# Kernel tuning notes

Hardware: AMD Instinct MI355X
Metric: run time of the kernel (lower is better)

Reference implementation:

```python
import jax, jax.numpy as jnp
import numpy as np

B, S, A, M, H, OUT = 256, 256, 256, 256, 8, 256
KD = A // H   # key_dim per head = 32
VD = M // H   # value_dim per head = 32


def setup_inputs() -> dict:
    key = jax.random.key(0)
    ks = jax.random.split(key, 11)
    return {
        "q_data": jax.random.normal(ks[0], (B, S, A), dtype=jnp.float32),
        "m_data": jax.random.normal(ks[1], (B, S, M), dtype=jnp.float32),
        "bias": jax.random.normal(ks[2], (B, 1, 1, S), dtype=jnp.float32),
        "nonbatched_bias": jax.random.normal(ks[3], (H, S, S), dtype=jnp.float32),
        "query_w": jax.random.normal(ks[4], (A, H, KD), dtype=jnp.float32) * 0.05,
        "key_w": jax.random.normal(ks[5], (M, H, KD), dtype=jnp.float32) * 0.05,
        "value_w": jax.random.normal(ks[6], (M, H, VD), dtype=jnp.float32) * 0.05,
        "gating_w": jax.random.normal(ks[7], (A, H, VD), dtype=jnp.float32) * 0.05,
        "gating_b": jax.random.normal(ks[8], (H, VD), dtype=jnp.float32) * 0.05,
        "output_w": jax.random.normal(ks[9], (H, VD, OUT), dtype=jnp.float32) * 0.05,
        "output_b": jax.random.normal(ks[10], (OUT,), dtype=jnp.float32) * 0.05,
    }


def reference(q_data, m_data, bias, nonbatched_bias,
              query_w, key_w, value_w, gating_w, gating_b, output_w, output_b):
    key_dim = query_w.shape[-1]
    # projections
    q = jnp.einsum('bqa,ahc->bqhc', q_data, query_w) * key_dim ** (-0.5)
    k = jnp.einsum('bka,ahc->bkhc', m_data, key_w)
    v = jnp.einsum('bka,ahc->bkhc', m_data, value_w)
    # logits [b,h,q,k] with batched + shared bias
    logits = jnp.einsum('bqhc,bkhc->bhqk', q, k) + bias + nonbatched_bias[None]
    weights = jax.nn.softmax(logits, axis=-1)
    weighted_avg = jnp.einsum('bhqk,bkhc->bqhc', weights, v)
    # sigmoid gating
    gate_values = jax.nn.sigmoid(jnp.einsum('bqc,chv->bqhv', q_data, gating_w) + gating_b)
    weighted_avg = weighted_avg * gate_values
    # output projection
    output = jnp.einsum('bqhc,hco->bqo', weighted_avg, output_w) + output_b
    return output
```

## Files before the change

kernel.cpp:

```cpp
#include <hip/hip_runtime.h>

typedef unsigned short u16;
typedef __attribute__((ext_vector_type(8))) short short8;
typedef __attribute__((ext_vector_type(4))) float f32x4;
typedef __attribute__((ext_vector_type(4))) unsigned int u32x4;
typedef __attribute__((ext_vector_type(4))) unsigned short u16x4;

#define LOG2E 1.4426950408889634f

__device__ __forceinline__ float bf2f(u16 u) {
    union { float f; unsigned int i; } c; c.i = ((unsigned int)u) << 16; return c.f;
}
__device__ __forceinline__ u16 f2bf(float f) {
    unsigned int x = __float_as_uint(f);
    x += 0x7fff + ((x >> 16) & 1);
    return (u16)(x >> 16);
}

union Cvt32 { u32x4 v[4]; u16 u[32]; };

__device__ __forceinline__ void ld32f_bf(const float* __restrict__ p, Cvt32& t) {
#pragma unroll
    for (int j = 0; j < 32; j += 4) {
        f32x4 x = *(const f32x4*)(p + j);
        t.u[j]     = f2bf(x[0]);
        t.u[j + 1] = f2bf(x[1]);
        t.u[j + 2] = f2bf(x[2]);
        t.u[j + 3] = f2bf(x[3]);
    }
}


__global__ __launch_bounds__(256) void prep_a(
    const float* __restrict__ nb,
    const float* __restrict__ qw, const float* __restrict__ kw,
    const float* __restrict__ vw, const float* __restrict__ gw,
    const float* __restrict__ ow,
    u16* __restrict__ wt, u16* __restrict__ WoT, u16* __restrict__ nbT)
{
    __shared__ float tile[64][65];
    int blk = blockIdx.x, tid = threadIdx.x;
    if (blk < 1024) {
        int e = blk * 256 + tid;
        int n = e & 255, k = (e >> 8) & 255, g = e >> 16;
        const float* W = g == 0 ? kw : g == 1 ? vw : g == 2 ? qw : gw;
        wt[(((g << 8) | n) << 8) | k] = f2bf(W[k * 256 + n]);
    } else if (blk < 1280) {
        int e = (blk - 1024) * 256 + tid;
        int o = e & 255, hc = e >> 8;
        WoT[o * 256 + hc] = f2bf(ow[hc * 256 + o]);
    } else {
        int idx = blk - 1280;
        int q0 = (idx & 3) * 64, k0 = ((idx >> 2) & 3) * 64, h = idx >> 4;
        int rr = tid >> 4;
        int cc = (tid & 15) << 2;
        const float* src = nb + ((size_t)(h * 256 + q0)) * 256 + k0;
#pragma unroll
        for (int p = 0; p < 4; p++) {
            int q = rr + p * 16;
            f32x4 x = *(const f32x4*)(src + (size_t)q * 256 + cc);
            tile[q][cc] = x[0]; tile[q][cc + 1] = x[1];
            tile[q][cc + 2] = x[2]; tile[q][cc + 3] = x[3];
        }
        __syncthreads();
        u16* dst = nbT + ((size_t)(h * 256 + k0)) * 256 + q0;
#pragma unroll
        for (int p = 0; p < 4; p++) {
            int k = rr + p * 16;
            u16x4 o;
#pragma unroll
            for (int u = 0; u < 4; u++) o[u] = f2bf(tile[cc + u][k] * LOG2E);
            *(u16x4*)(dst + (size_t)k * 256 + cc) = o;
        }
    }
}

__global__ __launch_bounds__(256) void proj_a(
    const float* __restrict__ m_data, const float* __restrict__ q_data,
    const u16* __restrict__ wt,
    u16* __restrict__ Kh, u16* __restrict__ Vh, u16* __restrict__ Qh,
    u16* __restrict__ GW, const float* __restrict__ gb)
{
    __shared__ u16 As[128 * 40];
    __shared__ u16 Bs[128 * 40];
    int bid = blockIdx.x;
    int xcd = bid & 7;
    int slot = bid >> 3;
    int y = slot & 7;
    int x = ((slot >> 3) << 3) | xcd;
    int row0 = x * 128;
    int n0 = y * 128;
    int g = y >> 1;
    const float* X = (g < 2) ? m_data : q_data;

    int tid = threadIdx.x;
    int lane = tid & 63, w = tid >> 6;
    int wm = w >> 1, wn = w & 1;
    int lr = tid >> 1;
    int lc = (tid & 1) << 4;

    const f32x4 fz = {0.f, 0.f, 0.f, 0.f};
    f32x4 acc[4][4];
#pragma unroll
    for (int i = 0; i < 4; i++)
#pragma unroll
        for (int j = 0; j < 4; j++) acc[i][j] = fz;

    int kl = (lane >> 4) << 3;
    int l15 = lane & 15;
    int rm = wm * 64 + l15;
    int rn = wn * 64 + l15;

    for (int kb = 0; kb < 8; ++kb) {
        int k0 = kb << 5;
        const float* pa = X + (size_t)(row0 + lr) * 256 + k0 + lc;
        f32x4 x0 = *(const f32x4*)pa;
        f32x4 x1 = *(const f32x4*)(pa + 4);
        f32x4 x2 = *(const f32x4*)(pa + 8);
        f32x4 x3 = *(const f32x4*)(pa + 12);
        union { u32x4 v[2]; u16 u[16]; } am;
        am.u[0] = f2bf(x0[0]); am.u[1] = f2bf(x0[1]); am.u[2] = f2bf(x0[2]); am.u[3] = f2bf(x0[3]);
        am.u[4] = f2bf(x1[0]); am.u[5] = f2bf(x1[1]); am.u[6] = f2bf(x1[2]); am.u[7] = f2bf(x1[3]);
        am.u[8] = f2bf(x2[0]); am.u[9] = f2bf(x2[1]); am.u[10] = f2bf(x2[2]); am.u[11] = f2bf(x2[3]);
        am.u[12] = f2bf(x3[0]); am.u[13] = f2bf(x3[1]); am.u[14] = f2bf(x3[2]); am.u[15] = f2bf(x3[3]);
        const u16* pb = wt + ((size_t)(n0 + lr) << 8) + k0 + lc;
        u32x4 b0 = *(const u32x4*)pb;
        u32x4 b1 = *(const u32x4*)(pb + 8);
        if (kb) __syncthreads();
        *(u32x4*)&As[lr * 40 + lc] = am.v[0];
        *(u32x4*)&As[lr * 40 + lc + 8] = am.v[1];
        *(u32x4*)&Bs[lr * 40 + lc] = b0;
        *(u32x4*)&Bs[lr * 40 + lc + 8] = b1;
        __syncthreads();
        short8 af[4], bf[4];
#pragma unroll
        for (int i = 0; i < 4; i++) af[i] = *(const short8*)&As[(rm + i * 16) * 40 + kl];
#pragma unroll
        for (int i = 0; i < 4; i++) bf[i] = *(const short8*)&Bs[(rn + i * 16) * 40 + kl];
#pragma unroll
        for (int mi = 0; mi < 4; mi++)
#pragma unroll
            for (int ni = 0; ni < 4; ni++)
                acc[mi][ni] = __builtin_amdgcn_mfma_f32_16x16x32_bf16(af[mi], bf[ni], acc[mi][ni], 0, 0, 0);
    }

    u16* dst = (g == 0) ? Kh : (g == 1) ? Vh : (g == 2) ? Qh : GW;
    float scale = (g == 2) ? 0.17677669529663687f * LOG2E : 1.f;
#pragma unroll
    for (int mi = 0; mi < 4; mi++)
#pragma unroll
        for (int ni = 0; ni < 4; ni++)
#pragma unroll
            for (int r = 0; r < 4; r++) {
                int row = row0 + wm * 64 + mi * 16 + ((lane >> 4) << 2) + r;
                int col = n0 + wn * 64 + ni * 16 + l15;
                float v = acc[mi][ni][r] * scale;
                int hc = col & 255;
                if (g == 3) v = (v + gb[hc]) * LOG2E;
                int b = row >> 8, s = row & 255, h = hc >> 5, c = col & 31;
                dst[((((size_t)b * 8 + h) << 8) + s) * 32 + c] = f2bf(v);
            }
}

__global__ __launch_bounds__(256, 3) void attn_a(
    const u16* __restrict__ Qh, const u16* __restrict__ Kh,
    const u16* __restrict__ Vh, u16* GW,
    const float* __restrict__ bias2, const u16* __restrict__ nbT)
{
    __shared__ u16 smem[23296];
    u16* Ksh = smem;
    u16* Vt  = smem + 10240;
    int bid = blockIdx.x;
    int b = bid >> 3, h = bid & 7;
    int tid = threadIdx.x, lane = tid & 63, w = tid >> 6;
    int l15 = lane & 15;
    int kl = (lane >> 4) << 3;
    int rq = (lane >> 4) << 2;
    size_t hoff = ((size_t)(b * 8 + h)) << 13;
    const f32x4 fz = {0.f, 0.f, 0.f, 0.f};
    u16* myP = smem + 18688 + w * 1152;

    {
        const u16* p = Kh + hoff + (tid << 5);
        u32x4 v0 = *(const u32x4*)p,        v1 = *(const u32x4*)(p + 8);
        u32x4 v2 = *(const u32x4*)(p + 16), v3 = *(const u32x4*)(p + 24);
        *(u32x4*)&Ksh[tid * 40] = v0;      *(u32x4*)&Ksh[tid * 40 + 8] = v1;
        *(u32x4*)&Ksh[tid * 40 + 16] = v2; *(u32x4*)&Ksh[tid * 40 + 24] = v3;
    }
    {
        const u16* p = Vh + hoff + (tid << 5);
        Cvt32 tm;
        tm.v[0] = *(const u32x4*)p;        tm.v[1] = *(const u32x4*)(p + 8);
        tm.v[2] = *(const u32x4*)(p + 16); tm.v[3] = *(const u32x4*)(p + 24);
#pragma unroll
        for (int c = 0; c < 32; c++) Vt[c * 264 + tid] = tm.u[c];
    }
    float bload[16];
#pragma unroll
    for (int t = 0; t < 16; t++)
        bload[t] = bias2[(b << 8) + t * 16 + l15] * LOG2E;
    __syncthreads();

    short8 kf[16];
#pragma unroll
    for (int t = 0; t < 16; t++) kf[t] = *(const short8*)&Ksh[(t * 16 + l15) * 40 + kl];

    const u16* nbh = nbT + ((size_t)h << 16);
    int orow = lane >> 2, ocol = (lane & 3) << 3;

#pragma unroll 1
    for (int mt = 0; mt < 4; ++mt) {
        int q0 = 64 * w + mt * 16 + rq;
        short8 qf = *(const short8*)(Qh + hoff + (size_t)(64 * w + mt * 16 + l15) * 32 + kl);

        size_t gaddr = hoff + (size_t)(64 * w + mt * 16 + orow) * 32 + ocol;
        u32x4 gl = *(const u32x4*)(GW + gaddr);

        const u16* nbp = nbh + q0;
        float srow[4] = {0.f, 0.f, 0.f, 0.f};
        f32x4 oacc[2] = {fz, fz};
#pragma unroll
        for (int qt = 0; qt < 4; ++qt) {
            f32x4 sc[4];
#pragma unroll
            for (int t = 0; t < 4; t++) {
                int tt = qt * 4 + t;
                f32x4 cb = {bload[tt], bload[tt], bload[tt], bload[tt]};
                sc[t] = __builtin_amdgcn_mfma_f32_16x16x32_bf16(qf, kf[tt], cb, 0, 0, 0);
            }
#pragma unroll
            for (int t = 0; t < 4; t++) {
                int tt = qt * 4 + t;
                u16x4 nbv = *(const u16x4*)(nbp + ((tt * 16 + l15) << 8));
#pragma unroll
                for (int r = 0; r < 4; r++) {
                    float p = __builtin_amdgcn_exp2f(sc[t][r] + bf2f(nbv[r]));
                    srow[r] += p;
                    myP[(rq + r) * 72 + t * 16 + l15] = f2bf(p);
                }
            }
#pragma unroll
            for (int ks = 0; ks < 2; ++ks) {
                short8 pf = *(const short8*)&myP[l15 * 72 + ks * 32 + kl];
#pragma unroll
                for (int ni = 0; ni < 2; ++ni) {
                    short8 vf = *(const short8*)&Vt[(ni * 16 + l15) * 264 + qt * 64 + ks * 32 + kl];
                    oacc[ni] = __builtin_amdgcn_mfma_f32_16x16x32_bf16(pf, vf, oacc[ni], 0, 0, 0);
                }
            }
        }
#pragma unroll
        for (int r = 0; r < 4; r++) {
            float s = srow[r];
            s += __shfl_xor(s, 1);
            s += __shfl_xor(s, 2);
            s += __shfl_xor(s, 4);
            s += __shfl_xor(s, 8);
            srow[r] = __builtin_amdgcn_rcpf(s);
        }

#pragma unroll
        for (int ni = 0; ni < 2; ++ni)
#pragma unroll
            for (int r = 0; r < 4; r++)
                myP[(rq + r) * 40 + ni * 16 + l15] = f2bf(oacc[ni][r] * srow[r]);
        u32x4 ov = *(const u32x4*)&myP[orow * 40 + ocol];
        union { u32x4 v; u16 u[8]; } oi, gi, oo;
        oi.v = ov; gi.v = gl;
#pragma unroll
        for (int j = 0; j < 8; j++) {
            float gate = __builtin_amdgcn_rcpf(1.f + __builtin_amdgcn_exp2f(-bf2f(gi.u[j])));
            oo.u[j] = f2bf(bf2f(oi.u[j]) * gate);
        }
        *(u32x4*)(GW + gaddr) = oo.v;
    }
}

__global__ __launch_bounds__(256) void gemmout_a(
    const u16* __restrict__ WA, const u16* __restrict__ WoT,
    float* __restrict__ dst, const float* __restrict__ ob)
{
    __shared__ u16 As[128 * 40];
    __shared__ u16 Bs[128 * 40];
    int tid = threadIdx.x;
    int lane = tid & 63, w = tid >> 6;
    int wm = w >> 1, wn = w & 1;
    int row0 = blockIdx.x * 128;
    int n0 = blockIdx.y * 128;
    int bq = row0 >> 8, s0 = row0 & 255;
    int lr = tid >> 1;
    int lc = (tid & 1) << 4;

    const f32x4 fz = {0.f, 0.f, 0.f, 0.f};
    f32x4 acc[4][4];
#pragma unroll
    for (int i = 0; i < 4; i++)
#pragma unroll
        for (int j = 0; j < 4; j++) acc[i][j] = fz;

    int kl = (lane >> 4) << 3;
    int l15 = lane & 15;
    int rm = wm * 64 + l15;
    int rn = wn * 64 + l15;

    for (int kb = 0; kb < 8; ++kb) {
        int k0 = kb << 5;
        const u16* pa = WA + ((((size_t)bq * 8 + kb) << 8) + s0 + lr) * 32 + lc;
        u32x4 a0 = *(const u32x4*)pa;
        u32x4 a1 = *(const u32x4*)(pa + 8);
        const u16* pb = WoT + ((size_t)(n0 + lr) << 8) + k0 + lc;
        u32x4 b0 = *(const u32x4*)pb;
        u32x4 b1 = *(const u32x4*)(pb + 8);
        if (kb) __syncthreads();
        *(u32x4*)&As[lr * 40 + lc] = a0;
        *(u32x4*)&As[lr * 40 + lc + 8] = a1;
        *(u32x4*)&Bs[lr * 40 + lc] = b0;
        *(u32x4*)&Bs[lr * 40 + lc + 8] = b1;
        __syncthreads();
        short8 af[4], bf[4];
#pragma unroll
        for (int i = 0; i < 4; i++) af[i] = *(const short8*)&As[(rm + i * 16) * 40 + kl];
#pragma unroll
        for (int i = 0; i < 4; i++) bf[i] = *(const short8*)&Bs[(rn + i * 16) * 40 + kl];
#pragma unroll
        for (int mi = 0; mi < 4; mi++)
#pragma unroll
            for (int ni = 0; ni < 4; ni++)
                acc[mi][ni] = __builtin_amdgcn_mfma_f32_16x16x32_bf16(af[mi], bf[ni], acc[mi][ni], 0, 0, 0);
    }

#pragma unroll
    for (int mi = 0; mi < 4; mi++)
#pragma unroll
        for (int ni = 0; ni < 4; ni++)
#pragma unroll
            for (int r = 0; r < 4; r++) {
                int row = row0 + wm * 64 + mi * 16 + ((lane >> 4) << 2) + r;
                int col = n0 + wn * 64 + ni * 16 + l15;
                dst[((size_t)row << 8) + col] = acc[mi][ni][r] + ob[col];
            }
}


__global__ __launch_bounds__(256) void transpose_k(
    const float* __restrict__ query_w, const float* __restrict__ key_w,
    const float* __restrict__ value_w, const float* __restrict__ gating_w,
    u16* __restrict__ wt)
{
    int i = blockIdx.x * 256 + threadIdx.x;
    int half = i >> 17;
    int rem = i & 131071;
    int h = rem >> 14, e = rem & 16383;
    int n = e >> 8, k = e & 255;
    int src_idx = k * 256 + h * 32 + (n & 31);
    float v;
    if (half == 0) v = (n < 32) ? key_w[src_idx]   : value_w[src_idx];
    else           v = (n < 32) ? query_w[src_idx] : gating_w[src_idx];
    wt[i] = f2bf(v);
}

__global__ __launch_bounds__(256) void fused_attn_k(
    const float* __restrict__ q_data, const float* __restrict__ m_data,
    const float* __restrict__ bias2, const float* __restrict__ nb,
    const u16* __restrict__ wt, const float* __restrict__ gb,
    u16* __restrict__ WAo)
{
    __shared__ u16 smem[31488];
    u16* Ksh = smem;
    u16* Vt  = smem + 10240;
    u16* Xs  = smem + 18688;
    u16* Wsh = smem + 28928;

    int bid = blockIdx.x;
    int b = bid >> 3, h = bid & 7;
    int tid = threadIdx.x, lane = tid & 63, w = tid >> 6;
    int l15 = lane & 15;
    int kl = (lane >> 4) << 3;
    int rq = (lane >> 4) << 2;
    const f32x4 fz = {0.f, 0.f, 0.f, 0.f};

    float bload[16];
#pragma unroll
    for (int t = 0; t < 16; t++) bload[t] = bias2[(b << 8) + t * 16 + l15];
    float gbc0 = gb[h * 32 + l15];
    float gbc1 = gb[h * 32 + 16 + l15];

    const float* Xg = m_data + ((size_t)b << 16);
    const u16* Wg = wt + (h << 14);
    f32x4 acc[4][4];
#pragma unroll
    for (int i = 0; i < 4; i++)
#pragma unroll
        for (int j = 0; j < 4; j++) acc[i][j] = fz;

    for (int kb = 0; kb < 8; ++kb) {
        Cvt32 am;
        ld32f_bf(Xg + (size_t)tid * 256 + kb * 32, am);
        u32x4 b0, b1;
        int nrow = tid >> 1, nc = (tid & 1) << 4;
        if (tid < 128) {
            const u16* q = Wg + nrow * 256 + kb * 32 + nc;
            b0 = *(const u32x4*)q; b1 = *(const u32x4*)(q + 8);
        }
        if (kb) __syncthreads();
        *(u32x4*)&Xs[tid * 40]      = am.v[0];
        *(u32x4*)&Xs[tid * 40 + 8]  = am.v[1];
        *(u32x4*)&Xs[tid * 40 + 16] = am.v[2];
        *(u32x4*)&Xs[tid * 40 + 24] = am.v[3];
        if (tid < 128) {
            *(u32x4*)&Wsh[nrow * 40 + nc] = b0;
            *(u32x4*)&Wsh[nrow * 40 + nc + 8] = b1;
        }
        __syncthreads();
        short8 af[4], bf[4];
#pragma unroll
        for (int i = 0; i < 4; i++) af[i] = *(const short8*)&Xs[(64 * w + i * 16 + l15) * 40 + kl];
#pragma unroll
        for (int i = 0; i < 4; i++) bf[i] = *(const short8*)&Wsh[(i * 16 + l15) * 40 + kl];
#pragma unroll
        for (int mi = 0; mi < 4; mi++)
#pragma unroll
            for (int ni = 0; ni < 4; ni++)
                acc[mi][ni] = __builtin_amdgcn_mfma_f32_16x16x32_bf16(af[mi], bf[ni], acc[mi][ni], 0, 0, 0);
    }
#pragma unroll
    for (int mi = 0; mi < 4; mi++)
#pragma unroll
        for (int ni = 0; ni < 4; ni++)
#pragma unroll
            for (int r = 0; r < 4; r++) {
                int s = 64 * w + mi * 16 + rq + r;
                int col = ni * 16 + l15;
                u16 v = f2bf(acc[mi][ni][r]);
                if (ni < 2) Ksh[s * 40 + col] = v;
                else        Vt[(col - 32) * 264 + s] = v;
            }
    __syncthreads();

    const float* Xg2 = q_data + ((size_t)b << 16);
    const u16* Wg2 = wt + 131072 + (h << 14);
    f32x4 acc2[4][4];
#pragma unroll
    for (int i = 0; i < 4; i++)
#pragma unroll
        for (int j = 0; j < 4; j++) acc2[i][j] = fz;

    for (int kb = 0; kb < 8; ++kb) {
        Cvt32 am;
        ld32f_bf(Xg2 + (size_t)tid * 256 + kb * 32, am);
        u32x4 b0, b1;
        int nrow = tid >> 1, nc = (tid & 1) << 4;
        if (tid < 128) {
            const u16* q = Wg2 + nrow * 256 + kb * 32 + nc;
            b0 = *(const u32x4*)q; b1 = *(const u32x4*)(q + 8);
        }
        __syncthreads();
        *(u32x4*)&Xs[tid * 40]      = am.v[0];
        *(u32x4*)&Xs[tid * 40 + 8]  = am.v[1];
        *(u32x4*)&Xs[tid * 40 + 16] = am.v[2];
        *(u32x4*)&Xs[tid * 40 + 24] = am.v[3];
        if (tid < 128) {
            *(u32x4*)&Wsh[nrow * 40 + nc] = b0;
            *(u32x4*)&Wsh[nrow * 40 + nc + 8] = b1;
        }
        __syncthreads();
        short8 af[4], bf[4];
#pragma unroll
        for (int i = 0; i < 4; i++) af[i] = *(const short8*)&Xs[(64 * w + i * 16 + l15) * 40 + kl];
#pragma unroll
        for (int i = 0; i < 4; i++) bf[i] = *(const short8*)&Wsh[(i * 16 + l15) * 40 + kl];
#pragma unroll
        for (int mi = 0; mi < 4; mi++)
#pragma unroll
            for (int ni = 0; ni < 4; ni++)
                acc2[mi][ni] = __builtin_amdgcn_mfma_f32_16x16x32_bf16(af[mi], bf[ni], acc2[mi][ni], 0, 0, 0);
    }
    __syncthreads();

    u16* myQ = smem + 18688 + w * 2816;
    u16* myP = myQ + 640;
    const float* nbp = nb + ((size_t)h << 16);
    const float qscale = 0.17677669529663687f;

#pragma unroll 1
    for (int mt = 0; mt < 4; ++mt) {
#pragma unroll
        for (int ni = 0; ni < 2; ++ni)
#pragma unroll
            for (int r = 0; r < 4; r++)
                myQ[(rq + r) * 40 + ni * 16 + l15] = f2bf(acc2[mt][ni][r] * qscale);

        short8 qf = *(const short8*)&myQ[l15 * 40 + kl];
        f32x4 sc[16];
#pragma unroll
        for (int t = 0; t < 16; t++) {
            short8 kfr = *(const short8*)&Ksh[(t * 16 + l15) * 40 + kl];
            sc[t] = __builtin_amdgcn_mfma_f32_16x16x32_bf16(qf, kfr, fz, 0, 0, 0);
        }

        int q0 = 64 * w + mt * 16 + rq;
        float mrow[4] = {-3e30f, -3e30f, -3e30f, -3e30f};
#pragma unroll
        for (int t = 0; t < 16; t++) {
            int kidx = t * 16 + l15;
#pragma unroll
            for (int r = 0; r < 4; r++) {
                float v = sc[t][r] + bload[t] + nbp[(size_t)(q0 + r) * 256 + kidx];
                sc[t][r] = v;
                mrow[r] = fmaxf(mrow[r], v);
            }
        }
#pragma unroll
        for (int r = 0; r < 4; r++) {
            float m = mrow[r];
            m = fmaxf(m, __shfl_xor(m, 1));
            m = fmaxf(m, __shfl_xor(m, 2));
            m = fmaxf(m, __shfl_xor(m, 4));
            m = fmaxf(m, __shfl_xor(m, 8));
            mrow[r] = m;
        }
        float srow[4] = {0.f, 0.f, 0.f, 0.f};
#pragma unroll
        for (int t = 0; t < 16; t++)
#pragma unroll
            for (int r = 0; r < 4; r++) {
                float p = __expf(sc[t][r] - mrow[r]);
                sc[t][r] = p;
                srow[r] += p;
            }
#pragma unroll
        for (int r = 0; r < 4; r++) {
            float s = srow[r];
            s += __shfl_xor(s, 1);
            s += __shfl_xor(s, 2);
            s += __shfl_xor(s, 4);
            s += __shfl_xor(s, 8);
            srow[r] = 1.f / s;
        }

        f32x4 oacc[2] = {fz, fz};
#pragma unroll
        for (int half = 0; half < 2; ++half) {
#pragma unroll
            for (int t = 0; t < 8; t++)
#pragma unroll
                for (int r = 0; r < 4; r++)
                    myP[(rq + r) * 136 + t * 16 + l15] =
                        f2bf(sc[half * 8 + t][r] * srow[r]);
#pragma unroll
            for (int ks = 0; ks < 4; ++ks) {
                short8 pf = *(const short8*)&myP[l15 * 136 + ks * 32 + kl];
#pragma unroll
                for (int ni = 0; ni < 2; ++ni) {
                    short8 vf = *(const short8*)&Vt[(ni * 16 + l15) * 264 + half * 128 + ks * 32 + kl];
                    oacc[ni] = __builtin_amdgcn_mfma_f32_16x16x32_bf16(pf, vf, oacc[ni], 0, 0, 0);
                }
            }
        }

#pragma unroll
        for (int ni = 0; ni < 2; ++ni) {
            float gbv = ni ? gbc1 : gbc0;
#pragma unroll
            for (int r = 0; r < 4; r++) {
                float gate = 1.f / (1.f + __expf(-(acc2[mt][ni + 2][r] + gbv)));
                size_t idx = (((size_t)b << 8) + q0 + r) * 256 + h * 32 + ni * 16 + l15;
                WAo[idx] = f2bf(oacc[ni][r] * gate);
            }
        }
    }
}

__global__ __launch_bounds__(256) void gemm_out_k(
    const u16* __restrict__ X, const float* __restrict__ Wo,
    float* __restrict__ dst, const float* __restrict__ cbias)
{
    __shared__ u16 As[128 * 40];
    __shared__ u16 Bs[128 * 40];
    int tid = threadIdx.x;
    int lane = tid & 63, w = tid >> 6;
    int wm = w >> 1, wn = w & 1;
    int row0 = blockIdx.x * 128;
    int n0 = blockIdx.y * 128;
    int lr = tid >> 1;
    int lc = (tid & 1) << 4;

    const f32x4 fz = {0.f, 0.f, 0.f, 0.f};
    f32x4 acc[4][4];
#pragma unroll
    for (int i = 0; i < 4; i++)
#pragma unroll
        for (int j = 0; j < 4; j++) acc[i][j] = fz;

    int kl = (lane >> 4) << 3;
    int l15 = lane & 15;
    int rm = wm * 64 + l15;
    int rn = wn * 64 + l15;

    for (int kb = 0; kb < 8; ++kb) {
        int k0 = kb << 5;
        const u16* pa = X + ((size_t)(row0 + lr) << 8) + k0 + lc;
        u32x4 a0 = *(const u32x4*)pa;
        u32x4 a1 = *(const u32x4*)(pa + 8);
        int bk = tid >> 3, bn = (tid & 7) << 4;
        const float* pb = Wo + (size_t)(k0 + bk) * 256 + n0 + bn;
        u16 bu[16];
#pragma unroll
        for (int j = 0; j < 16; j += 4) {
            f32x4 x = *(const f32x4*)(pb + j);
            bu[j] = f2bf(x[0]); bu[j + 1] = f2bf(x[1]);
            bu[j + 2] = f2bf(x[2]); bu[j + 3] = f2bf(x[3]);
        }
        if (kb) __syncthreads();
        *(u32x4*)&As[lr * 40 + lc] = a0;
        *(u32x4*)&As[lr * 40 + lc + 8] = a1;
#pragma unroll
        for (int j = 0; j < 16; j++) Bs[(bn + j) * 40 + bk] = bu[j];
        __syncthreads();
        short8 af[4], bf[4];
#pragma unroll
        for (int i = 0; i < 4; i++) af[i] = *(const short8*)&As[(rm + i * 16) * 40 + kl];
#pragma unroll
        for (int i = 0; i < 4; i++) bf[i] = *(const short8*)&Bs[(rn + i * 16) * 40 + kl];
#pragma unroll
        for (int mi = 0; mi < 4; mi++)
#pragma unroll
            for (int ni = 0; ni < 4; ni++)
                acc[mi][ni] = __builtin_amdgcn_mfma_f32_16x16x32_bf16(af[mi], bf[ni], acc[mi][ni], 0, 0, 0);
    }

#pragma unroll
    for (int mi = 0; mi < 4; mi++)
#pragma unroll
        for (int ni = 0; ni < 4; ni++)
#pragma unroll
            for (int r = 0; r < 4; r++) {
                int row = row0 + wm * 64 + mi * 16 + ((lane >> 4) << 2) + r;
                int col = n0 + wn * 64 + ni * 16 + l15;
                dst[((size_t)row << 8) + col] = acc[mi][ni][r] + cbias[col];
            }
}

extern "C" void kernel_launch(void* const* d_in, const int* in_sizes, int n_in,
                              void* d_out, int out_size, void* d_ws, size_t ws_size,
                              hipStream_t stream)
{
    const float* q_data   = (const float*)d_in[0];
    const float* m_data   = (const float*)d_in[1];
    const float* bias     = (const float*)d_in[2];
    const float* nb       = (const float*)d_in[3];
    const float* query_w  = (const float*)d_in[4];
    const float* key_w    = (const float*)d_in[5];
    const float* value_w  = (const float*)d_in[6];
    const float* gating_w = (const float*)d_in[7];
    const float* gating_b = (const float*)d_in[8];
    const float* output_w = (const float*)d_in[9];
    const float* output_b = (const float*)d_in[10];

    const size_t NEED_A = 4ull * 33554432 + 524288 + 131072 + 1048576;

    if (ws_size >= NEED_A) {
        u16* ws   = (u16*)d_ws;
        u16* Kh   = ws;
        u16* Vh   = Kh + 16777216;
        u16* Qh   = Vh + 16777216;
        u16* GW   = Qh + 16777216;
        u16* wt   = GW + 16777216;
        u16* WoT  = wt + 262144;
        u16* nbT  = WoT + 65536;

        prep_a<<<1408, 256, 0, stream>>>(nb, query_w, key_w, value_w, gating_w,
                                         output_w, wt, WoT, nbT);
        proj_a<<<4096, 256, 0, stream>>>(m_data, q_data, wt, Kh, Vh, Qh, GW, gating_b);
        attn_a<<<2048, 256, 0, stream>>>(Qh, Kh, Vh, GW, bias, nbT);
        gemmout_a<<<dim3(512, 2), 256, 0, stream>>>(GW, WoT, (float*)d_out, output_b);
    } else {
        u16* WAb = (u16*)d_ws;
        u16* wt  = (u16*)d_out;
        transpose_k<<<1024, 256, 0, stream>>>(query_w, key_w, value_w, gating_w, wt);
        fused_attn_k<<<2048, 256, 0, stream>>>(q_data, m_data, bias, nb, wt, gating_b, WAb);
        gemm_out_k<<<dim3(512, 2), 256, 0, stream>>>(WAb, output_w, (float*)d_out, output_b);
    }
}
```

Baseline: 441.9 us.

## Widen proj GEMM K-step, use packed bf16 convert, stage epilogue via LDS

The projection GEMM kernel now loads 64-wide K slices per iteration (4 iterations instead of 8), halving the barriers. The fp32-to-bf16 conversion of activations uses the packed v_cvt_pk_bf16_f32 instruction instead of manual rounding. The output epilogue writes results into shared memory first, then emits coalesced 16-byte stores per head row instead of scattered 2-byte stores. This cuts global store transactions and ALU work, at the cost of more LDS usage (36KB), which may lower occupancy.

```diff
diff --git a/kernel.cpp b/kernel.cpp
--- a/kernel.cpp
+++ b/kernel.cpp
@@ -15,6 +15,11 @@
     unsigned int x = __float_as_uint(f);
     x += 0x7fff + ((x >> 16) & 1);
     return (u16)(x >> 16);
+}
+__device__ __forceinline__ unsigned int cvtpk(float lo, float hi) {
+    unsigned int d;
+    asm("v_cvt_pk_bf16_f32 %0, %1, %2" : "=v"(d) : "v"(lo), "v"(hi));
+    return d;
 }
 
 union Cvt32 { u32x4 v[4]; u16 u[32]; };
@@ -81,8 +86,9 @@
     u16* __restrict__ Kh, u16* __restrict__ Vh, u16* __restrict__ Qh,
     u16* __restrict__ GW, const float* __restrict__ gb)
 {
-    __shared__ u16 As[128 * 40];
-    __shared__ u16 Bs[128 * 40];
+    __shared__ u16 smem[18432];
+    u16* As = smem;
+    u16* Bs = smem + 9216;
     int bid = blockIdx.x;
     int xcd = bid & 7;
     int slot = bid >> 3;
@@ -97,7 +103,7 @@
     int lane = tid & 63, w = tid >> 6;
     int wm = w >> 1, wn = w & 1;
     int lr = tid >> 1;
-    int lc = (tid & 1) << 4;
+    int lc2 = (tid & 1) << 5;
 
     const f32x4 fz = {0.f, 0.f, 0.f, 0.f};
     f32x4 acc[4][4];
@@ -108,58 +114,87 @@
 
     int kl = (lane >> 4) << 3;
     int l15 = lane & 15;
+    int rq = (lane >> 4) << 2;
     int rm = wm * 64 + l15;
     int rn = wn * 64 + l15;
 
-    for (int kb = 0; kb < 8; ++kb) {
-        int k0 = kb << 5;
-        const float* pa = X + (size_t)(row0 + lr) * 256 + k0 + lc;
-        f32x4 x0 = *(const f32x4*)pa;
-        f32x4 x1 = *(const f32x4*)(pa + 4);
-        f32x4 x2 = *(const f32x4*)(pa + 8);
-        f32x4 x3 = *(const f32x4*)(pa + 12);
-        union { u32x4 v[2]; u16 u[16]; } am;
-        am.u[0] = f2bf(x0[0]); am.u[1] = f2bf(x0[1]); am.u[2] = f2bf(x0[2]); am.u[3] = f2bf(x0[3]);
-        am.u[4] = f2bf(x1[0]); am.u[5] = f2bf(x1[1]); am.u[6] = f2bf(x1[2]); am.u[7] = f2bf(x1[3]);
-        am.u[8] = f2bf(x2[0]); am.u[9] = f2bf(x2[1]); am.u[10] = f2bf(x2[2]); am.u[11] = f2bf(x2[3]);
-        am.u[12] = f2bf(x3[0]); am.u[13] = f2bf(x3[1]); am.u[14] = f2bf(x3[2]); am.u[15] = f2bf(x3[3]);
-        const u16* pb = wt + ((size_t)(n0 + lr) << 8) + k0 + lc;
+    for (int kb = 0; kb < 4; ++kb) {
+        int k0 = kb << 6;
+        const float* pa = X + (size_t)(row0 + lr) * 256 + k0 + lc2;
+        union { u32x4 v[2]; unsigned int i[8]; } a0, a1;
+#pragma unroll
+        for (int j = 0; j < 4; j++) {
+            f32x4 xx = *(const f32x4*)(pa + j * 4);
+            a0.i[j * 2]     = cvtpk(xx[0], xx[1]);
+            a0.i[j * 2 + 1] = cvtpk(xx[2], xx[3]);
+        }
+#pragma unroll
+        for (int j = 0; j < 4; j++) {
+            f32x4 xx = *(const f32x4*)(pa + 16 + j * 4);
+            a1.i[j * 2]     = cvtpk(xx[0], xx[1]);
+            a1.i[j * 2 + 1] = cvtpk(xx[2], xx[3]);
+        }
+        const u16* pb = wt + ((size_t)(n0 + lr) << 8) + k0 + lc2;
         u32x4 b0 = *(const u32x4*)pb;
         u32x4 b1 = *(const u32x4*)(pb + 8);
+        u32x4 b2 = *(const u32x4*)(pb + 16);
+        u32x4 b3 = *(const u32x4*)(pb + 24);
         if (kb) __syncthreads();
-        *(u32x4*)&As[lr * 40 + lc] = am.v[0];
-        *(u32x4*)&As[lr * 40 + lc + 8] = am.v[1];
-        *(u32x4*)&Bs[lr * 40 + lc] = b0;
-        *(u32x4*)&Bs[lr * 40 + lc + 8] = b1;
+        *(u32x4*)&As[lr * 72 + lc2]      = a0.v[0];
+        *(u32x4*)&As[lr * 72 + lc2 + 8]  = a0.v[1];
+        *(u32x4*)&As[lr * 72 + lc2 + 16] = a1.v[0];
+        *(u32x4*)&As[lr * 72 + lc2 + 24] = a1.v[1];
+        *(u32x4*)&Bs[lr * 72 + lc2]      = b0;
+        *(u32x4*)&Bs[lr * 72 + lc2 + 8]  = b1;
+        *(u32x4*)&Bs[lr * 72 + lc2 + 16] = b2;
+        *(u32x4*)&Bs[lr * 72 + lc2 + 24] = b3;
         __syncthreads();
-        short8 af[4], bf[4];
-#pragma unroll
-        for (int i = 0; i < 4; i++) af[i] = *(const short8*)&As[(rm + i * 16) * 40 + kl];
-#pragma unroll
-        for (int i = 0; i < 4; i++) bf[i] = *(const short8*)&Bs[(rn + i * 16) * 40 + kl];
-#pragma unroll
-        for (int mi = 0; mi < 4; mi++)
-#pragma unroll
-            for (int ni = 0; ni < 4; ni++)
-                acc[mi][ni] = __builtin_amdgcn_mfma_f32_16x16x32_bf16(af[mi], bf[ni], acc[mi][ni], 0, 0, 0);
+#pragma unroll
+        for (int ks = 0; ks < 2; ++ks) {
+            short8 af[4], bf[4];
+#pragma unroll
+            for (int i = 0; i < 4; i++) af[i] = *(const short8*)&As[(rm + i * 16) * 72 + ks * 32 + kl];
+#pragma unroll
+            for (int i = 0; i < 4; i++) bf[i] = *(const short8*)&Bs[(rn + i * 16) * 72 + ks * 32 + kl];
+#pragma unroll
+            for (int mi = 0; mi < 4; mi++)
+#pragma unroll
+                for (int ni = 0; ni < 4; ni++)
+                    acc[mi][ni] = __builtin_amdgcn_mfma_f32_16x16x32_bf16(af[mi], bf[ni], acc[mi][ni], 0, 0, 0);
+        }
     }
 
     u16* dst = (g == 0) ? Kh : (g == 1) ? Vh : (g == 2) ? Qh : GW;
     float scale = (g == 2) ? 0.17677669529663687f * LOG2E : 1.f;
+
+    __syncthreads();
+    u16* Cs = smem;
 #pragma unroll
     for (int mi = 0; mi < 4; mi++)
 #pragma unroll
         for (int ni = 0; ni < 4; ni++)
 #pragma unroll
             for (int r = 0; r < 4; r++) {
-                int row = row0 + wm * 64 + mi * 16 + ((lane >> 4) << 2) + r;
-                int col = n0 + wn * 64 + ni * 16 + l15;
+                int row = wm * 64 + mi * 16 + rq + r;
+                int col = wn * 64 + ni * 16 + l15;
                 float v = acc[mi][ni][r] * scale;
-                int hc = col & 255;
-                if (g == 3) v = (v + gb[hc]) * LOG2E;
-                int b = row >> 8, s = row & 255, h = hc >> 5, c = col & 31;
-                dst[((((size_t)b * 8 + h) << 8) + s) * 32 + c] = f2bf(v);
-            }
+                if (g == 3) v = (v + gb[((y & 1) << 7) + col]) * LOG2E;
+                Cs[row * 136 + col] = f2bf(v);
+            }
+    __syncthreads();
+    {
+        int b = row0 >> 8, s0 = row0 & 255;
+        int hh = ((y & 1) << 2) | w;
+        u16* dstp = dst + ((((size_t)b * 8 + hh) << 8) + s0) * 32;
+        int ls = lane >> 2;
+        int lcc = (lane & 3) << 3;
+#pragma unroll
+        for (int p = 0; p < 8; p++) {
+            int s = p * 16 + ls;
+            u32x4 vv = *(const u32x4*)&Cs[s * 136 + w * 32 + lcc];
+            *(u32x4*)(dstp + (size_t)s * 32 + lcc) = vv;
+        }
+    }
 }
 
 __global__ __launch_bounds__(256, 3) void attn_a(
```

Result: slower. 463.8 us (+5.0%).

## Load MFMA fragments directly from global memory in projection and output GEMMs

Applied to the files above, without the earlier changes.

The projection and output GEMM kernels no longer stage A/B tiles through shared memory with two barriers per k-step. Each wave now loads its MFMA operand fragments straight from global memory, relying on L1/L2 for the reuse between waves. The fp32-to-bf16 conversion uses the packed v_cvt_pk_bf16_f32 instruction instead of manual rounding. This removes the LDS traffic and synchronisation, but each element is fetched by more waves and the global access pattern is less coalesced.

```diff
diff --git a/kernel.cpp b/kernel.cpp
--- a/kernel.cpp
+++ b/kernel.cpp
@@ -15,6 +15,11 @@
     unsigned int x = __float_as_uint(f);
     x += 0x7fff + ((x >> 16) & 1);
     return (u16)(x >> 16);
+}
+__device__ __forceinline__ unsigned int cvtpk(float lo, float hi) {
+    unsigned int d;
+    asm("v_cvt_pk_bf16_f32 %0, %1, %2" : "=v"(d) : "v"(lo), "v"(hi));
+    return d;
 }
 
 union Cvt32 { u32x4 v[4]; u16 u[32]; };
@@ -81,8 +86,6 @@
     u16* __restrict__ Kh, u16* __restrict__ Vh, u16* __restrict__ Qh,
     u16* __restrict__ GW, const float* __restrict__ gb)
 {
-    __shared__ u16 As[128 * 40];
-    __shared__ u16 Bs[128 * 40];
     int bid = blockIdx.x;
     int xcd = bid & 7;
     int slot = bid >> 3;
@@ -96,8 +99,6 @@
     int tid = threadIdx.x;
     int lane = tid & 63, w = tid >> 6;
     int wm = w >> 1, wn = w & 1;
-    int lr = tid >> 1;
-    int lc = (tid & 1) << 4;
 
     const f32x4 fz = {0.f, 0.f, 0.f, 0.f};
     f32x4 acc[4][4];
@@ -108,35 +109,29 @@
 
     int kl = (lane >> 4) << 3;
     int l15 = lane & 15;
-    int rm = wm * 64 + l15;
-    int rn = wn * 64 + l15;
-
+    int rq = (lane >> 4) << 2;
+
+    const float* pa = X + (size_t)(row0 + wm * 64 + l15) * 256 + kl;
+    const u16*   pb = wt + (size_t)(n0 + wn * 64 + l15) * 256 + kl;
+
+#pragma unroll 1
     for (int kb = 0; kb < 8; ++kb) {
         int k0 = kb << 5;
-        const float* pa = X + (size_t)(row0 + lr) * 256 + k0 + lc;
-        f32x4 x0 = *(const f32x4*)pa;
-        f32x4 x1 = *(const f32x4*)(pa + 4);
-        f32x4 x2 = *(const f32x4*)(pa + 8);
-        f32x4 x3 = *(const f32x4*)(pa + 12);
-        union { u32x4 v[2]; u16 u[16]; } am;
-        am.u[0] = f2bf(x0[0]); am.u[1] = f2bf(x0[1]); am.u[2] = f2bf(x0[2]); am.u[3] = f2bf(x0[3]);
-        am.u[4] = f2bf(x1[0]); am.u[5] = f2bf(x1[1]); am.u[6] = f2bf(x1[2]); am.u[7] = f2bf(x1[3]);
-        am.u[8] = f2bf(x2[0]); am.u[9] = f2bf(x2[1]); am.u[10] = f2bf(x2[2]); am.u[11] = f2bf(x2[3]);
-        am.u[12] = f2bf(x3[0]); am.u[13] = f2bf(x3[1]); am.u[14] = f2bf(x3[2]); am.u[15] = f2bf(x3[3]);
-        const u16* pb = wt + ((size_t)(n0 + lr) << 8) + k0 + lc;
-        u32x4 b0 = *(const u32x4*)pb;
-        u32x4 b1 = *(const u32x4*)(pb + 8);
-        if (kb) __syncthreads();
-        *(u32x4*)&As[lr * 40 + lc] = am.v[0];
-        *(u32x4*)&As[lr * 40 + lc + 8] = am.v[1];
-        *(u32x4*)&Bs[lr * 40 + lc] = b0;
-        *(u32x4*)&Bs[lr * 40 + lc + 8] = b1;
-        __syncthreads();
         short8 af[4], bf[4];
 #pragma unroll
-        for (int i = 0; i < 4; i++) af[i] = *(const short8*)&As[(rm + i * 16) * 40 + kl];
-#pragma unroll
-        for (int i = 0; i < 4; i++) bf[i] = *(const short8*)&Bs[(rn + i * 16) * 40 + kl];
+        for (int i = 0; i < 4; i++) {
+            f32x4 x0 = *(const f32x4*)(pa + (size_t)i * 16 * 256 + k0);
+            f32x4 x1 = *(const f32x4*)(pa + (size_t)i * 16 * 256 + k0 + 4);
+            union { unsigned int i4[4]; short8 s; } c;
+            c.i4[0] = cvtpk(x0[0], x0[1]);
+            c.i4[1] = cvtpk(x0[2], x0[3]);
+            c.i4[2] = cvtpk(x1[0], x1[1]);
+            c.i4[3] = cvtpk(x1[2], x1[3]);
+            af[i] = c.s;
+        }
+#pragma unroll
+        for (int i = 0; i < 4; i++)
+            bf[i] = *(const short8*)(pb + (size_t)i * 16 * 256 + k0);
 #pragma unroll
         for (int mi = 0; mi < 4; mi++)
 #pragma unroll
@@ -152,7 +147,7 @@
         for (int ni = 0; ni < 4; ni++)
 #pragma unroll
             for (int r = 0; r < 4; r++) {
-                int row = row0 + wm * 64 + mi * 16 + ((lane >> 4) << 2) + r;
+                int row = row0 + wm * 64 + mi * 16 + rq + r;
                 int col = n0 + wn * 64 + ni * 16 + l15;
                 float v = acc[mi][ni][r] * scale;
                 int hc = col & 255;
@@ -280,16 +275,12 @@
     const u16* __restrict__ WA, const u16* __restrict__ WoT,
     float* __restrict__ dst, const float* __restrict__ ob)
 {
-    __shared__ u16 As[128 * 40];
-    __shared__ u16 Bs[128 * 40];
     int tid = threadIdx.x;
     int lane = tid & 63, w = tid >> 6;
     int wm = w >> 1, wn = w & 1;
     int row0 = blockIdx.x * 128;
     int n0 = blockIdx.y * 128;
     int bq = row0 >> 8, s0 = row0 & 255;
-    int lr = tid >> 1;
-    int lc = (tid & 1) << 4;
 
     const f32x4 fz = {0.f, 0.f, 0.f, 0.f};
     f32x4 acc[4][4];
@@ -300,28 +291,20 @@
 
     int kl = (lane >> 4) << 3;
     int l15 = lane & 15;
-    int rm = wm * 64 + l15;
-    int rn = wn * 64 + l15;
-
+    int rq = (lane >> 4) << 2;
+
+    const u16* pb = WoT + (size_t)(n0 + wn * 64 + l15) * 256 + kl;
+
+#pragma unroll 1
     for (int kb = 0; kb < 8; ++kb) {
-        int k0 = kb << 5;
-        const u16* pa = WA + ((((size_t)bq * 8 + kb) << 8) + s0 + lr) * 32 + lc;
-        u32x4 a0 = *(const u32x4*)pa;
-        u32x4 a1 = *(const u32x4*)(pa + 8);
-        const u16* pb = WoT + ((size_t)(n0 + lr) << 8) + k0 + lc;
-        u32x4 b0 = *(const u32x4*)pb;
-        u32x4 b1 = *(const u32x4*)(pb + 8);
-        if (kb) __syncthreads();
-        *(u32x4*)&As[lr * 40 + lc] = a0;
-        *(u32x4*)&As[lr * 40 + lc + 8] = a1;
-        *(u32x4*)&Bs[lr * 40 + lc] = b0;
-        *(u32x4*)&Bs[lr * 40 + lc + 8] = b1;
-        __syncthreads();
         short8 af[4], bf[4];
 #pragma unroll
-        for (int i = 0; i < 4; i++) af[i] = *(const short8*)&As[(rm + i * 16) * 40 + kl];
-#pragma unroll
-        for (int i = 0; i < 4; i++) bf[i] = *(const short8*)&Bs[(rn + i * 16) * 40 + kl];
+        for (int i = 0; i < 4; i++)
+            af[i] = *(const short8*)(WA +
+                (((size_t)bq * 8 + kb) * 256 + s0 + wm * 64 + i * 16 + l15) * 32 + kl);
+#pragma unroll
+        for (int i = 0; i < 4; i++)
+            bf[i] = *(const short8*)(pb + (size_t)i * 16 * 256 + kb * 32);
 #pragma unroll
         for (int mi = 0; mi < 4; mi++)
 #pragma unroll
@@ -335,7 +318,7 @@
         for (int ni = 0; ni < 4; ni++)
 #pragma unroll
             for (int r = 0; r < 4; r++) {
-                int row = row0 + wm * 64 + mi * 16 + ((lane >> 4) << 2) + r;
+                int row = row0 + wm * 64 + mi * 16 + rq + r;
                 int col = n0 + wn * 64 + ni * 16 + l15;
                 dst[((size_t)row << 8) + col] = acc[mi][ni][r] + ob[col];
             }
```

After: 556.0 us. 1.26x slower.

## Stage full activation row-block in LDS once and reuse across four output tiles

Applied to the files above, without the earlier changes.

The projection kernel now loads a 128x256 slab of m_data or q_data once, converts it to bf16 with the packed v_cvt_pk_bf16_f32 instruction, and keeps it in LDS. It then loops over four 128-column output tiles, reading weight fragments directly from global memory. Before, each of the 4096 blocks re-read and re-converted its activation slice, so every fp32 input row was fetched four times. The grid drops to 1024 blocks and LDS use grows to about 66 KB per block, which reduces occupancy, and the weight loads move from LDS staging to direct global reads with no double buffering.

```diff
diff --git a/kernel.cpp b/kernel.cpp
--- a/kernel.cpp
+++ b/kernel.cpp
@@ -15,6 +15,11 @@
     unsigned int x = __float_as_uint(f);
     x += 0x7fff + ((x >> 16) & 1);
     return (u16)(x >> 16);
+}
+__device__ __forceinline__ unsigned int cvtpk(float lo, float hi) {
+    unsigned int d;
+    asm("v_cvt_pk_bf16_f32 %0, %1, %2" : "=v"(d) : "v"(lo), "v"(hi));
+    return d;
 }
 
 union Cvt32 { u32x4 v[4]; u16 u[32]; };
@@ -81,85 +86,84 @@
     u16* __restrict__ Kh, u16* __restrict__ Vh, u16* __restrict__ Qh,
     u16* __restrict__ GW, const float* __restrict__ gb)
 {
-    __shared__ u16 As[128 * 40];
-    __shared__ u16 Bs[128 * 40];
+    __shared__ u16 As[128 * 264];
     int bid = blockIdx.x;
-    int xcd = bid & 7;
-    int slot = bid >> 3;
-    int y = slot & 7;
-    int x = ((slot >> 3) << 3) | xcd;
+    int x = bid >> 1;
+    int src = bid & 1;
     int row0 = x * 128;
-    int n0 = y * 128;
-    int g = y >> 1;
-    const float* X = (g < 2) ? m_data : q_data;
+    const float* X = src ? q_data : m_data;
 
     int tid = threadIdx.x;
     int lane = tid & 63, w = tid >> 6;
     int wm = w >> 1, wn = w & 1;
-    int lr = tid >> 1;
-    int lc = (tid & 1) << 4;
-
-    const f32x4 fz = {0.f, 0.f, 0.f, 0.f};
-    f32x4 acc[4][4];
-#pragma unroll
-    for (int i = 0; i < 4; i++)
-#pragma unroll
-        for (int j = 0; j < 4; j++) acc[i][j] = fz;
-
     int kl = (lane >> 4) << 3;
     int l15 = lane & 15;
+    int rq = (lane >> 4) << 2;
+
+    {
+        const float* base = X + (size_t)row0 * 256;
+#pragma unroll
+        for (int it = 0; it < 32; ++it) {
+            int fi = (it * 256 + tid) * 4;
+            int row = fi >> 8, col = fi & 255;
+            f32x4 xx = *(const f32x4*)(base + fi);
+            union { unsigned int i2[2]; u16x4 s; } c;
+            c.i2[0] = cvtpk(xx[0], xx[1]);
+            c.i2[1] = cvtpk(xx[2], xx[3]);
+            *(u16x4*)&As[row * 264 + col] = c.s;
+        }
+    }
+    __syncthreads();
+
+    const f32x4 fz = {0.f, 0.f, 0.f, 0.f};
     int rm = wm * 64 + l15;
-    int rn = wn * 64 + l15;
-
-    for (int kb = 0; kb < 8; ++kb) {
-        int k0 = kb << 5;
-        const float* pa = X + (size_t)(row0 + lr) * 256 + k0 + lc;
-        f32x4 x0 = *(const f32x4*)pa;
-        f32x4 x1 = *(const f32x4*)(pa + 4);
-        f32x4 x2 = *(const f32x4*)(pa + 8);
-        f32x4 x3 = *(const f32x4*)(pa + 12);
-        union { u32x4 v[2]; u16 u[16]; } am;
-        am.u[0] = f2bf(x0[0]); am.u[1] = f2bf(x0[1]); am.u[2] = f2bf(x0[2]); am.u[3] = f2bf(x0[3]);
-        am.u[4] = f2bf(x1[0]); am.u[5] = f2bf(x1[1]); am.u[6] = f2bf(x1[2]); am.u[7] = f2bf(x1[3]);
-        am.u[8] = f2bf(x2[0]); am.u[9] = f2bf(x2[1]); am.u[10] = f2bf(x2[2]); am.u[11] = f2bf(x2[3]);
-        am.u[12] = f2bf(x3[0]); am.u[13] = f2bf(x3[1]); am.u[14] = f2bf(x3[2]); am.u[15] = f2bf(x3[3]);
-        const u16* pb = wt + ((size_t)(n0 + lr) << 8) + k0 + lc;
-        u32x4 b0 = *(const u32x4*)pb;
-        u32x4 b1 = *(const u32x4*)(pb + 8);
-        if (kb) __syncthreads();
-        *(u32x4*)&As[lr * 40 + lc] = am.v[0];
-        *(u32x4*)&As[lr * 40 + lc + 8] = am.v[1];
-        *(u32x4*)&Bs[lr * 40 + lc] = b0;
-        *(u32x4*)&Bs[lr * 40 + lc + 8] = b1;
-        __syncthreads();
-        short8 af[4], bf[4];
-#pragma unroll
-        for (int i = 0; i < 4; i++) af[i] = *(const short8*)&As[(rm + i * 16) * 40 + kl];
-#pragma unroll
-        for (int i = 0; i < 4; i++) bf[i] = *(const short8*)&Bs[(rn + i * 16) * 40 + kl];
+
+#pragma unroll 1
+    for (int nt = 0; nt < 4; ++nt) {
+        int n0 = src * 512 + nt * 128;
+        int g  = n0 >> 8;
+        const u16* pb = wt + (size_t)(n0 + wn * 64 + l15) * 256 + kl;
+
+        f32x4 acc[4][4];
+#pragma unroll
+        for (int i = 0; i < 4; i++)
+#pragma unroll
+            for (int j = 0; j < 4; j++) acc[i][j] = fz;
+
+#pragma unroll
+        for (int kb = 0; kb < 8; ++kb) {
+            int k0 = kb << 5;
+            short8 af[4], bf[4];
+#pragma unroll
+            for (int i = 0; i < 4; i++)
+                af[i] = *(const short8*)&As[(rm + i * 16) * 264 + k0 + kl];
+#pragma unroll
+            for (int i = 0; i < 4; i++)
+                bf[i] = *(const short8*)(pb + (size_t)i * 16 * 256 + k0);
+#pragma unroll
+            for (int mi = 0; mi < 4; mi++)
+#pragma unroll
+                for (int ni = 0; ni < 4; ni++)
+                    acc[mi][ni] = __builtin_amdgcn_mfma_f32_16x16x32_bf16(af[mi], bf[ni], acc[mi][ni], 0, 0, 0);
+        }
+
+        u16* dst = (g == 0) ? Kh : (g == 1) ? Vh : (g == 2) ? Qh : GW;
+        float scale = (g == 2) ? 0.17677669529663687f * LOG2E : 1.f;
 #pragma unroll
         for (int mi = 0; mi < 4; mi++)
 #pragma unroll
             for (int ni = 0; ni < 4; ni++)
-                acc[mi][ni] = __builtin_amdgcn_mfma_f32_16x16x32_bf16(af[mi], bf[ni], acc[mi][ni], 0, 0, 0);
-    }
-
-    u16* dst = (g == 0) ? Kh : (g == 1) ? Vh : (g == 2) ? Qh : GW;
-    float scale = (g == 2) ? 0.17677669529663687f * LOG2E : 1.f;
-#pragma unroll
-    for (int mi = 0; mi < 4; mi++)
-#pragma unroll
-        for (int ni = 0; ni < 4; ni++)
-#pragma unroll
-            for (int r = 0; r < 4; r++) {
-                int row = row0 + wm * 64 + mi * 16 + ((lane >> 4) << 2) + r;
-                int col = n0 + wn * 64 + ni * 16 + l15;
-                float v = acc[mi][ni][r] * scale;
-                int hc = col & 255;
-                if (g == 3) v = (v + gb[hc]) * LOG2E;
-                int b = row >> 8, s = row & 255, h = hc >> 5, c = col & 31;
-                dst[((((size_t)b * 8 + h) << 8) + s) * 32 + c] = f2bf(v);
-            }
+#pragma unroll
+                for (int r = 0; r < 4; r++) {
+                    int row = row0 + wm * 64 + mi * 16 + rq + r;
+                    int col = n0 + wn * 64 + ni * 16 + l15;
+                    float v = acc[mi][ni][r] * scale;
+                    int hc = col & 255;
+                    if (g == 3) v = (v + gb[hc]) * LOG2E;
+                    int b = row >> 8, s = row & 255, h = hc >> 5, c = col & 31;
+                    dst[((((size_t)b * 8 + h) << 8) + s) * 32 + c] = f2bf(v);
+                }
+    }
 }
 
 __global__ __launch_bounds__(256, 3) void attn_a(
@@ -671,7 +675,7 @@
 
         prep_a<<<1408, 256, 0, stream>>>(nb, query_w, key_w, value_w, gating_w,
                                          output_w, wt, WoT, nbT);
-        proj_a<<<4096, 256, 0, stream>>>(m_data, q_data, wt, Kh, Vh, Qh, GW, gating_b);
+        proj_a<<<1024, 256, 0, stream>>>(m_data, q_data, wt, Kh, Vh, Qh, GW, gating_b);
         attn_a<<<2048, 256, 0, stream>>>(Qh, Kh, Vh, GW, bias, nbT);
         gemmout_a<<<dim3(512, 2), 256, 0, stream>>>(GW, WoT, (float*)d_out, output_b);
     } else {
```

Result: slower. 476.6 us (+7.8%).
